# Optimization experiments

Measured on AMD Instinct MI355X. Metric: run time of the kernel, lower is better.

Reference implementation:

```python
import jax, jax.numpy as jnp
import numpy as np

LATENT_PACKET_SIZE = 16

def setup_inputs() -> dict:
    key = jax.random.key(0)
    z = jax.random.normal(key, (4096, 1, 8192), dtype=jnp.float32)
    return {"z": z}

def reference(z) -> jnp.ndarray:
    B = z.shape[0]
    D = z.shape[2]
    P = LATENT_PACKET_SIZE
    n_packets = D // P
    zp = z.reshape(B, n_packets, P)                      # (B, N, P)
    # sort packets within each sample by the first element of each packet
    inds = jnp.argsort(zp[:, :, 0], axis=1)              # (B, N) int
    z_ordered = jnp.take_along_axis(zp, inds[:, :, None], axis=1)  # batched gather
    return z_ordered.reshape(B, 1, n_packets * P)
```

## Files before the change

### kernel.cpp

```cpp
#include <hip/hip_runtime.h>


#define NPK 512
#define DIM 8192
#define NT  256
#define RPB 4

typedef float vfloat4 __attribute__((ext_vector_type(4)));

__device__ __forceinline__ unsigned int sx32(unsigned int x, int lj) {
    if (lj == 1)  return (unsigned int)__builtin_amdgcn_mov_dpp((int)x, 0xB1, 0xF, 0xF, true);
    if (lj == 2)  return (unsigned int)__builtin_amdgcn_mov_dpp((int)x, 0x4E, 0xF, 0xF, true);
    if (lj == 4)  return (unsigned int)__builtin_amdgcn_ds_swizzle((int)x, 0x101F);
    if (lj == 8)  return (unsigned int)__builtin_amdgcn_ds_swizzle((int)x, 0x201F);
    if (lj == 16) return (unsigned int)__builtin_amdgcn_ds_swizzle((int)x, 0x401F);
    return (unsigned int)__shfl_xor((int)x, lj);
}

__device__ __forceinline__ unsigned long long sx64(unsigned long long v, int lj) {
    const unsigned int lo = sx32((unsigned int)v, lj);
    const unsigned int hi = sx32((unsigned int)(v >> 32), lj);
    return ((unsigned long long)hi << 32) | lo;
}

__global__ __launch_bounds__(NT, 8)
void sort_latent_kernel(const float* __restrict__ z, float* __restrict__ out) {
    __shared__ int srcs[RPB][NPK];

    const int t    = threadIdx.x;
    const int w    = t >> 6;
    const int lane = t & 63;
    const size_t rowoff = ((size_t)blockIdx.x * RPB + w) * DIM;
    const float*  __restrict__ zrow = z + rowoff;
    const vfloat4* __restrict__ zin4 = (const vfloat4*)zrow;
    vfloat4* __restrict__ out4 = (vfloat4*)(out + rowoff);

    unsigned long long v[8];
#pragma unroll
    for (int s = 0; s < 8; ++s) {
        const int e = lane * 8 + s;
        unsigned int u = __float_as_uint(zrow[e * 16]);
        if (u == 0x80000000u) u = 0u;
        u = (u & 0x80000000u) ? ~u : (u | 0x80000000u);
        v[s] = ((unsigned long long)u << 16) | (unsigned long long)e;
    }

#pragma unroll
    for (int kk = 1; kk <= 9; ++kk) {
        const int k = 1 << kk;
#pragma unroll
        for (int jj = kk - 1; jj >= 0; --jj) {
            const int j = 1 << jj;
            if (j >= 8) {
                const int lj = j >> 3;
                const bool up = ((lane & (k >> 3)) == 0);
                const bool keep_min = (up == ((lane & lj) == 0));
#pragma unroll
                for (int s = 0; s < 8; ++s) {
                    const unsigned long long a  = v[s];
                    const unsigned long long vp = sx64(a, lj);
                    const bool lt = a < vp;
                    v[s] = (keep_min == lt) ? a : vp;
                }
            } else {
#pragma unroll
                for (int s = 0; s < 8; ++s) {
                    if ((s & j) == 0) {
                        const int p = s | j;
                        const bool up = ((((lane << 3) | s) & k) == 0);
                        const unsigned long long a = v[s], b = v[p];
                        const bool lt = a < b;
                        const bool do_swap = (lt != up);
                        v[s] = do_swap ? b : a;
                        v[p] = do_swap ? a : b;
                    }
                }
            }
        }
    }

#pragma unroll
    for (int s = 0; s < 8; ++s)
        srcs[w][lane * 8 + s] = (int)(v[s] & 0xffffull);

#pragma unroll 8
    for (int i = 0; i < DIM / 4 / 64; ++i) {
        const int o = i * 64 + lane;
        const int src = srcs[w][o >> 2];
        const vfloat4 val = zin4[src * 4 + (o & 3)];
        __builtin_nontemporal_store(val, &out4[o]);
    }
}

extern "C" void kernel_launch(void* const* d_in, const int* in_sizes, int n_in,
                              void* d_out, int out_size, void* d_ws, size_t ws_size,
                              hipStream_t stream) {
    const float* z = (const float*)d_in[0];
    float* out = (float*)d_out;
    const int nrows = in_sizes[0] / DIM;
    sort_latent_kernel<<<nrows / RPB, NT, 0, stream>>>(z, out);
}
```

Baseline: 254.6 us.

## Split sort and gather into separate kernels with a workspace permutation buffer

Sorting moves into its own kernel, which writes a 16-bit permutation per row to the workspace. A second kernel, using one block per row, reads that permutation and batches four 16-byte gathers before storing them. The goal is to stop the memory-bound gather from being serialized behind the register-heavy bitonic sort in each wave, so each phase can get its own occupancy. The cost is an extra launch and a second strided read of the key elements. If no workspace is available, the code falls back to a one-row-per-block kernel that sorts through shared memory.

```diff
diff --git a/kernel.cpp b/kernel.cpp
--- a/kernel.cpp
+++ b/kernel.cpp
@@ -3,10 +3,16 @@
 
 #define NPK 512
 #define DIM 8192
-#define NT  256
-#define RPB 4
 
 typedef float vfloat4 __attribute__((ext_vector_type(4)));
+typedef unsigned short vushort8 __attribute__((ext_vector_type(8)));
+
+
+__device__ __forceinline__ unsigned long long shfl_xor_u64(unsigned long long v, int mask) {
+    const int lo = __shfl_xor((int)(unsigned int)(v & 0xffffffffull), mask);
+    const int hi = __shfl_xor((int)(unsigned int)(v >> 32), mask);
+    return ((unsigned long long)(unsigned int)hi << 32) | (unsigned int)lo;
+}
 
 __device__ __forceinline__ unsigned int sx32(unsigned int x, int lj) {
     if (lj == 1)  return (unsigned int)__builtin_amdgcn_mov_dpp((int)x, 0xB1, 0xF, 0xF, true);
@@ -23,17 +29,14 @@
     return ((unsigned long long)hi << 32) | lo;
 }
 
-__global__ __launch_bounds__(NT, 8)
-void sort_latent_kernel(const float* __restrict__ z, float* __restrict__ out) {
-    __shared__ int srcs[RPB][NPK];
 
+__global__ __launch_bounds__(256, 8)
+void sort_keys_kernel(const float* __restrict__ z, unsigned short* __restrict__ perm) {
     const int t    = threadIdx.x;
     const int w    = t >> 6;
     const int lane = t & 63;
-    const size_t rowoff = ((size_t)blockIdx.x * RPB + w) * DIM;
-    const float*  __restrict__ zrow = z + rowoff;
-    const vfloat4* __restrict__ zin4 = (const vfloat4*)zrow;
-    vfloat4* __restrict__ out4 = (vfloat4*)(out + rowoff);
+    const int row  = blockIdx.x * 4 + w;
+    const float* __restrict__ zrow = z + (size_t)row * DIM;
 
     unsigned long long v[8];
 #pragma unroll
@@ -79,16 +82,95 @@
         }
     }
 
+    vushort8 pk;
 #pragma unroll
     for (int s = 0; s < 8; ++s)
-        srcs[w][lane * 8 + s] = (int)(v[s] & 0xffffull);
+        pk[s] = (unsigned short)(v[s] & 0xffffull);
+    ((vushort8*)(perm + (size_t)row * NPK))[lane] = pk;
+}
 
-#pragma unroll 8
-    for (int i = 0; i < DIM / 4 / 64; ++i) {
-        const int o = i * 64 + lane;
-        const int src = srcs[w][o >> 2];
-        const vfloat4 val = zin4[src * 4 + (o & 3)];
-        __builtin_nontemporal_store(val, &out4[o]);
+
+__global__ __launch_bounds__(256, 8)
+void gather_kernel(const float* __restrict__ z, const unsigned short* __restrict__ perm,
+                   float* __restrict__ out) {
+    __shared__ int srcs[NPK];
+
+    const int t = threadIdx.x;
+    const size_t rowoff = (size_t)blockIdx.x * DIM;
+    const vfloat4* __restrict__ zin4 = (const vfloat4*)(z + rowoff);
+    vfloat4* __restrict__ out4 = (vfloat4*)(out + rowoff);
+
+    const unsigned int* __restrict__ pr =
+        (const unsigned int*)(perm + (size_t)blockIdx.x * NPK);
+    const unsigned int wp = pr[t];
+    srcs[2 * t]     = (int)(wp & 0xffffu);
+    srcs[2 * t + 1] = (int)(wp >> 16);
+    __syncthreads();
+
+#pragma unroll
+    for (int g = 0; g < 2; ++g) {
+        int src[4];
+        vfloat4 val[4];
+#pragma unroll
+        for (int i = 0; i < 4; ++i)
+            src[i] = srcs[(t + 256 * (4 * g + i)) >> 2];
+#pragma unroll
+        for (int i = 0; i < 4; ++i) {
+            const int o = t + 256 * (4 * g + i);
+            val[i] = zin4[(src[i] << 2) | (o & 3)];
+        }
+        __builtin_amdgcn_sched_barrier(0);
+#pragma unroll
+        for (int i = 0; i < 4; ++i)
+            __builtin_nontemporal_store(val[i], &out4[t + 256 * (4 * g + i)]);
+    }
+}
+
+
+__global__ __launch_bounds__(512, 8)
+void sort_latent_kernel(const float* __restrict__ z, float* __restrict__ out) {
+    __shared__ __align__(16) unsigned long long keys[NPK];
+    __shared__ int srcs[NPK];
+
+    const int t = threadIdx.x;
+    const size_t rowoff = (size_t)blockIdx.x * DIM;
+    const float* __restrict__ zrow = z + rowoff;
+    const vfloat4* __restrict__ zin4 = (const vfloat4*)zrow;
+    vfloat4* __restrict__ out4 = (vfloat4*)(out + rowoff);
+
+    unsigned int u = __float_as_uint(zrow[t * 16]);
+    if (u == 0x80000000u) u = 0u;
+    u = (u & 0x80000000u) ? ~u : (u | 0x80000000u);
+    unsigned long long v = ((unsigned long long)u << 16) | (unsigned long long)t;
+
+#pragma unroll
+    for (int kk = 1; kk <= 9; ++kk) {
+        const int k = 1 << kk;
+#pragma unroll
+        for (int jj = kk - 1; jj >= 0; --jj) {
+            const int j = 1 << jj;
+            unsigned long long vp;
+            if (j < 64) {
+                vp = shfl_xor_u64(v, j);
+            } else {
+                __syncthreads();
+                keys[t] = v;
+                __syncthreads();
+                vp = keys[t ^ j];
+            }
+            const bool take_min = (((t & k) == 0) == ((t & j) == 0));
+            const bool lt = (v < vp);
+            v = (take_min == lt) ? v : vp;
+        }
+    }
+    srcs[t] = (int)(v & 0xffffull);
+    __syncthreads();
+
+#pragma unroll
+    for (int i = 0; i < 4; ++i) {
+        const int o = t + 512 * i;
+        const int src = srcs[o >> 2];
+        __builtin_nontemporal_store(zin4[(src << 2) | (o & 3)], &out4[o]);
     }
 }
 
@@ -98,5 +180,13 @@
     const float* z = (const float*)d_in[0];
     float* out = (float*)d_out;
     const int nrows = in_sizes[0] / DIM;
-    sort_latent_kernel<<<nrows / RPB, NT, 0, stream>>>(z, out);
+    const size_t perm_bytes = (size_t)nrows * NPK * sizeof(unsigned short);
+
+    if (d_ws != nullptr && ws_size >= perm_bytes) {
+        unsigned short* perm = (unsigned short*)d_ws;
+        sort_keys_kernel<<<nrows / 4, 256, 0, stream>>>(z, perm);
+        gather_kernel<<<nrows, 256, 0, stream>>>(z, perm, out);
+    } else {
+        sort_latent_kernel<<<nrows, 512, 0, stream>>>(z, out);
+    }
 }
```

Measured after the change: 257.6 us. About the same (+1.1%).
